# Performance work log

Measured on AMD Instinct MI355X. Metric: run time of the kernel, lower is better.

## Reference

```python
import jax, jax.numpy as jnp
import numpy as np
from jax import lax

KS = 3
PAD = 1


def setup_inputs() -> dict:
    key = jax.random.key(0)
    k1, k2, k3 = jax.random.split(key, 3)
    b, c, h, w = 8, 64, 128, 128
    out_c = 64
    x = jax.random.normal(k1, (b, c, h, w), dtype=jnp.float32)
    # small offset weights keep predicted offsets in a sane range
    w_off = jax.random.normal(k2, (2 * KS * KS, c, KS, KS), dtype=jnp.float32) * 0.05
    b_off = jnp.zeros((2 * KS * KS,), dtype=jnp.float32)
    w_reg = jax.random.normal(k3, (out_c, c * KS * KS), dtype=jnp.float32) * 0.02
    b_reg = jnp.zeros((out_c,), dtype=jnp.float32)
    return {"x": x, "w_off": w_off, "b_off": b_off, "w_reg": w_reg, "b_reg": b_reg}


def _deform_forward(x, w_off, b_off, w_reg, b_reg):
    ks, pad = KS, PAD
    b, c, h, w = x.shape
    # offset conv: 3x3, stride 1, pad 1 -> [b, 2*ks*ks, h, w]
    offset = lax.conv_general_dilated(
        x, w_off, window_strides=(1, 1), padding=[(pad, pad), (pad, pad)],
        dimension_numbers=("NCHW", "OIHW", "NCHW"))
    offset = offset + b_off[None, :, None, None]

    # pad input (zeros), as in the torch module
    xp = jnp.pad(x, ((0, 0), (0, 0), (pad, pad), (pad, pad)))
    Hp, Wp = h + 2 * pad, w + 2 * pad

    dt = x.dtype
    # base grid p0: [...,0] = column (x), [...,1] = row (y)
    yy, xx = jnp.meshgrid(jnp.arange(h, dtype=dt), jnp.arange(w, dtype=dt), indexing="ij")
    # kernel offsets p_n: flattened k = i*ks + j -> (lin[j], lin[i])
    lin = jnp.linspace(-(ks - 1) // 2, (ks - 1) // 2, ks).astype(dt)
    pn_i, pn_j = jnp.meshgrid(lin, lin, indexing="ij")
    pn = jnp.stack([pn_j, pn_i], axis=-1).reshape(ks * ks, 2)  # [ks2, 2]

    # offsets: [b, ks2, 2, h, w] -> [b, ks2, h, w, 2]; [...,0]=x off, [...,1]=y off
    off = offset.reshape(b, ks * ks, 2, h, w).transpose(0, 1, 3, 4, 2)

    px = xx[None, None] + pn[None, :, 0, None, None] + off[..., 0]  # [b, ks2, h, w]
    py = yy[None, None] + pn[None, :, 1, None, None] + off[..., 1]

    # torch normalizes by UNPADDED (w-1, h-1) but samples the PADDED tensor with
    # align_corners=True; reproduce exactly: q = p/(dim-1) * (dim_pad-1)
    qx = px / (w - 1) * (Wp - 1)
    qy = py / (h - 1) * (Hp - 1)

    x0 = jnp.floor(qx)
    y0 = jnp.floor(qy)
    wx1 = qx - x0  # frac weights
    wy1 = qy - y0
    wx0 = 1.0 - wx1
    wy0 = 1.0 - wy1
    ix0 = x0.astype(jnp.int32)
    iy0 = y0.astype(jnp.int32)
    ix1 = ix0 + 1
    iy1 = iy0 + 1

    def corner(iy, ix):
        valid = ((iy >= 0) & (iy < Hp) & (ix >= 0) & (ix < Wp)).astype(dt)
        iyc = jnp.clip(iy, 0, Hp - 1)
        ixc = jnp.clip(ix, 0, Wp - 1)
        # gather per batch: img [c,Hp,Wp], idx [ks2,h,w] -> [c,ks2,h,w]
        vals = jax.vmap(lambda img, a, bb: img[:, a, bb])(xp, iyc, ixc)
        return vals * valid[:, None]  # broadcast over channel dim

    v00 = corner(iy0, ix0)
    v01 = corner(iy0, ix1)
    v10 = corner(iy1, ix0)
    v11 = corner(iy1, ix1)

    wy0e = wy0[:, None]; wy1e = wy1[:, None]
    wx0e = wx0[:, None]; wx1e = wx1[:, None]
    sampled = (v00 * wy0e * wx0e + v01 * wy0e * wx1e +
               v10 * wy1e * wx0e + v11 * wy1e * wx1e)  # [b, c, ks2, h, w]

    # layout matches torch: [b, c*ks2, h, w] with (c, kk) order
    xs = sampled.reshape(b, c * ks * ks, h, w)
    out = jnp.einsum("bkhw,ok->bohw", xs, w_reg) + b_reg[None, :, None, None]
    return out


def reference(x, w_off, b_off, w_reg, b_reg):
    return _deform_forward(x, w_off, b_off, w_reg, b_reg)
```

## Files before the change

### kernel.cpp

```cpp
#include <hip/hip_runtime.h>
#include <math.h>

#define HH 128
#define WW 128
#define CC 64
#define BB 8
#define OC 64
#define OFFC 18
#define HW (HH*WW)
#define HP 136
#define WP 136
#define PHW (HP*WP)

typedef __attribute__((ext_vector_type(8))) _Float16 f16x8;
typedef __attribute__((ext_vector_type(4))) float f32x4;

#define P_OFF      0
#define P_SIZE     (BB*32*PHW)
#define OFFS_OFF   (P_OFF + P_SIZE)
#define OFFS_SIZE  (BB*OFFC*HW)
#define WAREG_OFF  (OFFS_OFF + OFFS_SIZE)
#define WAREG_SIZE 18432
#define WAOFF_OFF  (WAREG_OFF + WAREG_SIZE)

__device__ __forceinline__ unsigned short f2h(float f) {
    _Float16 t = (_Float16)f;
    unsigned short s;
    __builtin_memcpy(&s, &t, 2);
    return s;
}
__device__ __forceinline__ f16x8 u4_to_h8(uint4 u) {
    union { uint4 u; f16x8 h; } c; c.u = u; return c.h;
}
__device__ __forceinline__ uint4 h8_to_u4(f16x8 h) {
    union { uint4 u; f16x8 h; } c; c.h = h; return c.u;
}
__device__ __forceinline__ f16x8 splat8(float f) {
    _Float16 t = (_Float16)f;
    return (f16x8){t, t, t, t, t, t, t, t};
}

__global__ __launch_bounds__(256) void prep_kernel(
    const float* __restrict__ w_reg, const float* __restrict__ w_off,
    unsigned short* __restrict__ wA_reg, unsigned short* __restrict__ wA_off)
{
    int i = blockIdx.x * 256 + threadIdx.x;
    if (i < 18 * 64 * 32) {
        int j = i & 7, quad = (i >> 3) & 3, o = (i >> 5) & 63, ks = i >> 11;
        int kt = ks >> 1, kk = ks & 1;
        int c = kk * 32 + quad * 8 + j;
        wA_reg[i] = f2h(w_reg[o * 576 + c * 9 + kt]);
    }
    if (i < 18 * 32 * 32) {
        int j = i & 7, quad = (i >> 3) & 3, o = (i >> 5) & 31, ks = i >> 10;
        int kt = ks >> 1, kk = ks & 1;
        int c = kk * 32 + quad * 8 + j;
        float v = (o < OFFC) ? w_off[(o * CC + c) * 9 + kt] : 0.0f;
        wA_off[i] = f2h(v);
    }
}

__global__ __launch_bounds__(256) void pad_kernel(
    const float* __restrict__ x, uint4* __restrict__ P)
{
    int idx = blockIdx.x * 256 + threadIdx.x;
    if (idx >= BB * 8 * PHW) return;
    int pos = idx % PHW;
    int ig  = idx / PHW;
    int r   = pos / WP;
    int col = pos % WP;
    union { uint4 u; f16x8 h; } cv;
    cv.u = make_uint4(0u, 0u, 0u, 0u);
    if (r >= 4 && r <= 131 && col >= 4 && col <= 131) {
        const float* src = x + (ig * 8) * HW + (r - 4) * WW + (col - 4);
        #pragma unroll
        for (int e = 0; e < 8; ++e)
            cv.h[e] = (_Float16)src[e * HW];
    }
    P[idx] = cv.u;
}

__global__ __launch_bounds__(256) void offset_conv_kernel(
    const uint4* __restrict__ P, const unsigned short* __restrict__ wA_off,
    const float* __restrict__ b_off, float* __restrict__ offs)
{
    __shared__ uint4 xs[3 * 8 * 132];
    int img  = blockIdx.x & 7;
    int pblk = blockIdx.x >> 3;
    int tid  = threadIdx.x;
    const f16x8* wAv = (const f16x8*)wA_off;
    int lane = tid & 63;
    int wvid = tid >> 6;
    int s  = wvid & 1;
    int ph = wvid >> 1;

    for (int i = tid; i < 3 * 8 * 130; i += 256) {
        int r   = i / 1040;
        int rem = i - r * 1040;
        int g   = rem / 130;
        int j   = rem - g * 130;
        xs[(r * 8 + g) * 132 + j] =
            P[(img * 8 + g) * PHW + (pblk + 3 + r) * WP + (j + 3)];
    }
    __syncthreads();

    f32x4 acc[4];
    #pragma unroll
    for (int pt = 0; pt < 4; ++pt) acc[pt] = (f32x4){0.f, 0.f, 0.f, 0.f};

    const f16x8* xsv = (const f16x8*)xs;
    for (int tap = 0; tap < 9; ++tap) {
        int dy = tap / 3, dx = tap % 3;
        f16x8 a0 = wAv[((tap * 2 + 0) * 32 + s * 16 + (lane & 15)) * 4 + (lane >> 4)];
        f16x8 a1 = wAv[((tap * 2 + 1) * 32 + s * 16 + (lane & 15)) * 4 + (lane >> 4)];
        #pragma unroll
        for (int pt = 0; pt < 4; ++pt) {
            int j = ph * 64 + pt * 16 + (lane & 15) + dx;
            f16x8 b0 = xsv[(dy * 8 + (lane >> 4)) * 132 + j];
            acc[pt] = __builtin_amdgcn_mfma_f32_16x16x32_f16(a0, b0, acc[pt], 0, 0, 0);
            f16x8 b1 = xsv[(dy * 8 + 4 + (lane >> 4)) * 132 + j];
            acc[pt] = __builtin_amdgcn_mfma_f32_16x16x32_f16(a1, b1, acc[pt], 0, 0, 0);
        }
    }

    float* ob = offs + img * (OFFC * HW) + pblk * 128;
    #pragma unroll
    for (int r = 0; r < 4; ++r) {
        int o = s * 16 + (lane >> 4) * 4 + r;
        if (o < OFFC) {
            float bias = b_off[o];
            #pragma unroll
            for (int pt = 0; pt < 4; ++pt) {
                int pxl = ph * 64 + pt * 16 + (lane & 15);
                ob[o * HW + pxl] = acc[pt][r] + bias;
            }
        }
    }
}


struct Gather8 {
    uint4 a00, a01, a10, a11;
    uint4 b00, b01, b10, b11;
    float wx1, wy1;
};

__device__ __forceinline__ Gather8 issue_tap(
    const uint4* __restrict__ xq0, const uint4* __restrict__ xq1,
    int wv, int hv, int dx, int dy, float offx, float offy)
{
    const float scale = 129.0f / 127.0f;
    float pxf = ((float)wv + (float)dx) + offx;
    float pyf = ((float)hv + (float)dy) + offy;
    float qx = fminf(fmaxf(pxf * scale, -100.0f), 300.0f);
    float qy = fminf(fmaxf(pyf * scale, -100.0f), 300.0f);
    float x0f = floorf(qx), y0f = floorf(qy);
    Gather8 g;
    g.wx1 = qx - x0f;
    g.wy1 = qy - y0f;
    int ix0 = (int)x0f, iy0 = (int)y0f;
    int c0 = min(max(ix0 + 3, 0), WP - 2);
    int r0 = min(max(iy0 + 3, 0), HP - 1);
    int r1 = min(max(iy0 + 4, 0), HP - 1);
    int pr0 = r0 * WP + c0, pr1 = r1 * WP + c0;
    g.a00 = xq0[pr0]; g.a01 = xq0[pr0 + 1];
    g.a10 = xq0[pr1]; g.a11 = xq0[pr1 + 1];
    g.b00 = xq1[pr0]; g.b01 = xq1[pr0 + 1];
    g.b10 = xq1[pr1]; g.b11 = xq1[pr1 + 1];
    return g;
}

__device__ __forceinline__ void blend_write(
    uint4* __restrict__ dst, int qp, int pxl, const Gather8& g)
{
    f16x8 wx1v = splat8(g.wx1), wx0v = splat8(1.0f - g.wx1);
    f16x8 wy1v = splat8(g.wy1), wy0v = splat8(1.0f - g.wy1);
    f16x8 r0a = u4_to_h8(g.a00) * wx0v + u4_to_h8(g.a01) * wx1v;
    f16x8 r1a = u4_to_h8(g.a10) * wx0v + u4_to_h8(g.a11) * wx1v;
    dst[(qp * 2 + 0) * 64 + pxl] = h8_to_u4(r0a * wy0v + r1a * wy1v);
    f16x8 r0b = u4_to_h8(g.b00) * wx0v + u4_to_h8(g.b01) * wx1v;
    f16x8 r1b = u4_to_h8(g.b10) * wx0v + u4_to_h8(g.b11) * wx1v;
    dst[(qp * 2 + 1) * 64 + pxl] = h8_to_u4(r0b * wy0v + r1b * wy1v);
}

__global__ __launch_bounds__(256, 4) void deform_main_kernel(
    const uint4* __restrict__ P, const float* __restrict__ offs,
    const unsigned short* __restrict__ wA_reg, const float* __restrict__ b_reg,
    float* __restrict__ out)
{
    __shared__ uint4 xs2[2 * 512];
    int img  = blockIdx.x & 7;
    int rest = blockIdx.x >> 3;
    int half = rest & 1;
    int pblk = rest >> 1;
    int tid  = threadIdx.x;
    int pxl  = tid & 63;
    int qp   = tid >> 6;
    int wv = half * 64 + pxl;
    int hv = pblk;
    const float*  obf = offs + img * (OFFC * HW) + hv * WW + wv;
    const f16x8*  wAv = (const f16x8*)wA_reg;
    int lane = tid & 63;
    int wvid = tid >> 6;
    const uint4* xq0 = P + (img * 8 + qp * 2 + 0) * PHW;
    const uint4* xq1 = P + (img * 8 + qp * 2 + 1) * PHW;
    int aidx = (wvid * 16 + (lane & 15)) * 4 + (lane >> 4);

    f32x4 acc[4];
    #pragma unroll
    for (int pt = 0; pt < 4; ++pt) acc[pt] = (f32x4){0.f, 0.f, 0.f, 0.f};

    float ox0 = obf[0],      oy0 = obf[HW];
    float ox1 = obf[2 * HW], oy1 = obf[3 * HW];
    Gather8 cur = issue_tap(xq0, xq1, wv, hv, -1, -1, ox0, oy0);
    f16x8 a0c = wAv[0 * 64 * 4 + aidx];
    f16x8 a1c = wAv[1 * 64 * 4 + aidx];

    #pragma unroll
    for (int tap = 0; tap < 9; ++tap) {
        uint4* dst = xs2 + (tap & 1) * 512;
        blend_write(dst, qp, pxl, cur);

        float ox2 = 0.f, oy2 = 0.f;
        if (tap < 7) {
            ox2 = obf[(2 * tap + 4) * HW];
            oy2 = obf[(2 * tap + 5) * HW];
        }

        Gather8 nxt;
        f16x8 a0n, a1n;
        if (tap < 8) {
            int dx1 = (tap + 1) % 3 - 1, dy1 = (tap + 1) / 3 - 1;
            nxt = issue_tap(xq0, xq1, wv, hv, dx1, dy1, ox1, oy1);
            a0n = wAv[((tap + 1) * 2 + 0) * 64 * 4 + aidx];
            a1n = wAv[((tap + 1) * 2 + 1) * 64 * 4 + aidx];
        }

        asm volatile("s_waitcnt lgkmcnt(0)" ::: "memory");
        __builtin_amdgcn_s_barrier();
        asm volatile("" ::: "memory");

        const f16x8* xsv = (const f16x8*)(xs2 + (tap & 1) * 512);
        #pragma unroll
        for (int pt = 0; pt < 4; ++pt) {
            int pxi = pt * 16 + (lane & 15);
            f16x8 b0 = xsv[(lane >> 4) * 64 + pxi];
            acc[pt] = __builtin_amdgcn_mfma_f32_16x16x32_f16(a0c, b0, acc[pt], 0, 0, 0);
            f16x8 b1 = xsv[(4 + (lane >> 4)) * 64 + pxi];
            acc[pt] = __builtin_amdgcn_mfma_f32_16x16x32_f16(a1c, b1, acc[pt], 0, 0, 0);
        }

        if (tap < 8) {
            cur = nxt; a0c = a0n; a1c = a1n;
            ox1 = ox2; oy1 = oy2;
        }
    }

    float* op = out + img * (OC * HW) + hv * WW + half * 64;
    #pragma unroll
    for (int r = 0; r < 4; ++r) {
        int o = wvid * 16 + (lane >> 4) * 4 + r;
        float bias = b_reg[o];
        #pragma unroll
        for (int pt = 0; pt < 4; ++pt)
            op[o * HW + pt * 16 + (lane & 15)] = acc[pt][r] + bias;
    }
}

extern "C" void kernel_launch(void* const* d_in, const int* in_sizes, int n_in,
                              void* d_out, int out_size, void* d_ws, size_t ws_size,
                              hipStream_t stream) {
    const float* x     = (const float*)d_in[0];
    const float* w_off = (const float*)d_in[1];
    const float* b_off = (const float*)d_in[2];
    const float* w_reg = (const float*)d_in[3];
    const float* b_reg = (const float*)d_in[4];
    float* out = (float*)d_out;
    float* ws  = (float*)d_ws;

    uint4* P      = (uint4*)(ws + P_OFF);
    float* offs   = ws + OFFS_OFF;
    unsigned short* wA_reg = (unsigned short*)(ws + WAREG_OFF);
    unsigned short* wA_off = (unsigned short*)(ws + WAOFF_OFF);

    prep_kernel<<<144, 256, 0, stream>>>(w_reg, w_off, wA_reg, wA_off);
    pad_kernel<<<(BB * 8 * PHW + 255) / 256, 256, 0, stream>>>(x, P);
    offset_conv_kernel<<<1024, 256, 0, stream>>>(P, wA_off, b_off, offs);
    deform_main_kernel<<<2048, 256, 0, stream>>>(P, offs, wA_reg, b_reg, out);
}
```

Before: 155.1 us.

## Fuse offset conv into deform kernel and merge prep with pad kernel

Computes the offset convolution inside the deform kernel for each 64-pixel half-row, keeps the offsets in LDS and drops the global offs buffer. Also merges the weight-prep and pad kernels into a single launch. This removes two kernel launches and the global write and read of the offset tensor. In exchange each block stages its own input halo and does extra MFMA work with an added barrier, and LDS use per block goes up, which could limit occupancy.

```diff
diff --git a/kernel.cpp b/kernel.cpp
--- a/kernel.cpp
+++ b/kernel.cpp
@@ -23,6 +23,9 @@
 #define WAREG_SIZE 18432
 #define WAOFF_OFF  (WAREG_OFF + WAREG_SIZE)
 
+#define PAD_BLOCKS 4624
+#define PREP_BLOCKS 144
+
 __device__ __forceinline__ unsigned short f2h(float f) {
     _Float16 t = (_Float16)f;
     unsigned short s;
@@ -40,104 +43,45 @@
     return (f16x8){t, t, t, t, t, t, t, t};
 }
 
-__global__ __launch_bounds__(256) void prep_kernel(
+__global__ __launch_bounds__(256) void prep_pad_kernel(
+    const float* __restrict__ x, uint4* __restrict__ P,
     const float* __restrict__ w_reg, const float* __restrict__ w_off,
     unsigned short* __restrict__ wA_reg, unsigned short* __restrict__ wA_off)
 {
-    int i = blockIdx.x * 256 + threadIdx.x;
-    if (i < 18 * 64 * 32) {
-        int j = i & 7, quad = (i >> 3) & 3, o = (i >> 5) & 63, ks = i >> 11;
-        int kt = ks >> 1, kk = ks & 1;
-        int c = kk * 32 + quad * 8 + j;
-        wA_reg[i] = f2h(w_reg[o * 576 + c * 9 + kt]);
-    }
-    if (i < 18 * 32 * 32) {
-        int j = i & 7, quad = (i >> 3) & 3, o = (i >> 5) & 31, ks = i >> 10;
-        int kt = ks >> 1, kk = ks & 1;
-        int c = kk * 32 + quad * 8 + j;
-        float v = (o < OFFC) ? w_off[(o * CC + c) * 9 + kt] : 0.0f;
-        wA_off[i] = f2h(v);
-    }
-}
-
-__global__ __launch_bounds__(256) void pad_kernel(
-    const float* __restrict__ x, uint4* __restrict__ P)
-{
-    int idx = blockIdx.x * 256 + threadIdx.x;
-    if (idx >= BB * 8 * PHW) return;
-    int pos = idx % PHW;
-    int ig  = idx / PHW;
-    int r   = pos / WP;
-    int col = pos % WP;
-    union { uint4 u; f16x8 h; } cv;
-    cv.u = make_uint4(0u, 0u, 0u, 0u);
-    if (r >= 4 && r <= 131 && col >= 4 && col <= 131) {
-        const float* src = x + (ig * 8) * HW + (r - 4) * WW + (col - 4);
-        #pragma unroll
-        for (int e = 0; e < 8; ++e)
-            cv.h[e] = (_Float16)src[e * HW];
-    }
-    P[idx] = cv.u;
-}
-
-__global__ __launch_bounds__(256) void offset_conv_kernel(
-    const uint4* __restrict__ P, const unsigned short* __restrict__ wA_off,
-    const float* __restrict__ b_off, float* __restrict__ offs)
-{
-    __shared__ uint4 xs[3 * 8 * 132];
-    int img  = blockIdx.x & 7;
-    int pblk = blockIdx.x >> 3;
-    int tid  = threadIdx.x;
-    const f16x8* wAv = (const f16x8*)wA_off;
-    int lane = tid & 63;
-    int wvid = tid >> 6;
-    int s  = wvid & 1;
-    int ph = wvid >> 1;
-
-    for (int i = tid; i < 3 * 8 * 130; i += 256) {
-        int r   = i / 1040;
-        int rem = i - r * 1040;
-        int g   = rem / 130;
-        int j   = rem - g * 130;
-        xs[(r * 8 + g) * 132 + j] =
-            P[(img * 8 + g) * PHW + (pblk + 3 + r) * WP + (j + 3)];
-    }
-    __syncthreads();
-
-    f32x4 acc[4];
-    #pragma unroll
-    for (int pt = 0; pt < 4; ++pt) acc[pt] = (f32x4){0.f, 0.f, 0.f, 0.f};
-
-    const f16x8* xsv = (const f16x8*)xs;
-    for (int tap = 0; tap < 9; ++tap) {
-        int dy = tap / 3, dx = tap % 3;
-        f16x8 a0 = wAv[((tap * 2 + 0) * 32 + s * 16 + (lane & 15)) * 4 + (lane >> 4)];
-        f16x8 a1 = wAv[((tap * 2 + 1) * 32 + s * 16 + (lane & 15)) * 4 + (lane >> 4)];
-        #pragma unroll
-        for (int pt = 0; pt < 4; ++pt) {
-            int j = ph * 64 + pt * 16 + (lane & 15) + dx;
-            f16x8 b0 = xsv[(dy * 8 + (lane >> 4)) * 132 + j];
-            acc[pt] = __builtin_amdgcn_mfma_f32_16x16x32_f16(a0, b0, acc[pt], 0, 0, 0);
-            f16x8 b1 = xsv[(dy * 8 + 4 + (lane >> 4)) * 132 + j];
-            acc[pt] = __builtin_amdgcn_mfma_f32_16x16x32_f16(a1, b1, acc[pt], 0, 0, 0);
-        }
-    }
-
-    float* ob = offs + img * (OFFC * HW) + pblk * 128;
-    #pragma unroll
-    for (int r = 0; r < 4; ++r) {
-        int o = s * 16 + (lane >> 4) * 4 + r;
-        if (o < OFFC) {
-            float bias = b_off[o];
+    int bid = blockIdx.x;
+    int tid = threadIdx.x;
+    if (bid < PAD_BLOCKS) {
+        int idx = bid * 256 + tid;
+        int pos = idx % PHW;
+        int ig  = idx / PHW;
+        int r   = pos / WP;
+        int col = pos % WP;
+        union { uint4 u; f16x8 h; } cv;
+        cv.u = make_uint4(0u, 0u, 0u, 0u);
+        if (r >= 4 && r <= 131 && col >= 4 && col <= 131) {
+            const float* src = x + (ig * 8) * HW + (r - 4) * WW + (col - 4);
             #pragma unroll
-            for (int pt = 0; pt < 4; ++pt) {
-                int pxl = ph * 64 + pt * 16 + (lane & 15);
-                ob[o * HW + pxl] = acc[pt][r] + bias;
-            }
-        }
-    }
-}
-
+            for (int e = 0; e < 8; ++e)
+                cv.h[e] = (_Float16)src[e * HW];
+        }
+        P[idx] = cv.u;
+    } else {
+        int i = (bid - PAD_BLOCKS) * 256 + tid;
+        if (i < 18 * 64 * 32) {
+            int j = i & 7, quad = (i >> 3) & 3, o = (i >> 5) & 63, ks = i >> 11;
+            int kt = ks >> 1, kk = ks & 1;
+            int c = kk * 32 + quad * 8 + j;
+            wA_reg[i] = f2h(w_reg[o * 576 + c * 9 + kt]);
+        }
+        if (i < 18 * 32 * 32) {
+            int j = i & 7, quad = (i >> 3) & 3, o = (i >> 5) & 31, ks = i >> 10;
+            int kt = ks >> 1, kk = ks & 1;
+            int c = kk * 32 + quad * 8 + j;
+            float v = (o < OFFC) ? w_off[(o * CC + c) * 9 + kt] : 0.0f;
+            wA_off[i] = f2h(v);
+        }
+    }
+}
 
 struct Gather8 {
     uint4 a00, a01, a10, a11;
@@ -183,12 +127,13 @@
     dst[(qp * 2 + 1) * 64 + pxl] = h8_to_u4(r0b * wy0v + r1b * wy1v);
 }
 
-__global__ __launch_bounds__(256, 4) void deform_main_kernel(
-    const uint4* __restrict__ P, const float* __restrict__ offs,
-    const unsigned short* __restrict__ wA_reg, const float* __restrict__ b_reg,
-    float* __restrict__ out)
-{
-    __shared__ uint4 xs2[2 * 512];
+__global__ __launch_bounds__(256, 4) void fused_deform_kernel(
+    const uint4* __restrict__ P, const unsigned short* __restrict__ wA_off,
+    const float* __restrict__ b_off, const unsigned short* __restrict__ wA_reg,
+    const float* __restrict__ b_reg, float* __restrict__ out)
+{
+    __shared__ uint4 shbuf[3 * 8 * 66];
+    __shared__ float offs_lds[OFFC * 64];
     int img  = blockIdx.x & 7;
     int rest = blockIdx.x >> 3;
     int half = rest & 1;
@@ -196,12 +141,58 @@
     int tid  = threadIdx.x;
     int pxl  = tid & 63;
     int qp   = tid >> 6;
+    int lane = tid & 63;
+    int wvid = tid >> 6;
     int wv = half * 64 + pxl;
     int hv = pblk;
-    const float*  obf = offs + img * (OFFC * HW) + hv * WW + wv;
-    const f16x8*  wAv = (const f16x8*)wA_reg;
-    int lane = tid & 63;
-    int wvid = tid >> 6;
+
+    for (int i = tid; i < 3 * 8 * 66; i += 256) {
+        int r   = i / 528;
+        int rem = i - r * 528;
+        int g   = rem / 66;
+        int j   = rem - g * 66;
+        shbuf[(r * 8 + g) * 66 + j] =
+            P[(img * 8 + g) * PHW + (pblk + 3 + r) * WP + (half * 64 + 3 + j)];
+    }
+    __syncthreads();
+
+    {
+        int s2  = wvid & 1;
+        int ph2 = wvid >> 1;
+        const f16x8* wOv = (const f16x8*)wA_off;
+        const f16x8* xsc = (const f16x8*)shbuf;
+        f32x4 oacc[2];
+        oacc[0] = (f32x4){0.f, 0.f, 0.f, 0.f};
+        oacc[1] = (f32x4){0.f, 0.f, 0.f, 0.f};
+        for (int tap = 0; tap < 9; ++tap) {
+            int dy = tap / 3, dx = tap % 3;
+            f16x8 a0 = wOv[((tap * 2 + 0) * 32 + s2 * 16 + (lane & 15)) * 4 + (lane >> 4)];
+            f16x8 a1 = wOv[((tap * 2 + 1) * 32 + s2 * 16 + (lane & 15)) * 4 + (lane >> 4)];
+            #pragma unroll
+            for (int pt = 0; pt < 2; ++pt) {
+                int sj = ph2 * 32 + pt * 16 + (lane & 15) + dx;
+                f16x8 b0 = xsc[(dy * 8 + (lane >> 4)) * 66 + sj];
+                oacc[pt] = __builtin_amdgcn_mfma_f32_16x16x32_f16(a0, b0, oacc[pt], 0, 0, 0);
+                f16x8 b1 = xsc[(dy * 8 + 4 + (lane >> 4)) * 66 + sj];
+                oacc[pt] = __builtin_amdgcn_mfma_f32_16x16x32_f16(a1, b1, oacc[pt], 0, 0, 0);
+            }
+        }
+        #pragma unroll
+        for (int r = 0; r < 4; ++r) {
+            int o = s2 * 16 + (lane >> 4) * 4 + r;
+            if (o < OFFC) {
+                float bias = b_off[o];
+                #pragma unroll
+                for (int pt = 0; pt < 2; ++pt) {
+                    int p = ph2 * 32 + pt * 16 + (lane & 15);
+                    offs_lds[o * 64 + p] = oacc[pt][r] + bias;
+                }
+            }
+        }
+    }
+    __syncthreads();
+
+    const f16x8* wAv = (const f16x8*)wA_reg;
     const uint4* xq0 = P + (img * 8 + qp * 2 + 0) * PHW;
     const uint4* xq1 = P + (img * 8 + qp * 2 + 1) * PHW;
     int aidx = (wvid * 16 + (lane & 15)) * 4 + (lane >> 4);
@@ -210,37 +201,32 @@
     #pragma unroll
     for (int pt = 0; pt < 4; ++pt) acc[pt] = (f32x4){0.f, 0.f, 0.f, 0.f};
 
-    float ox0 = obf[0],      oy0 = obf[HW];
-    float ox1 = obf[2 * HW], oy1 = obf[3 * HW];
-    Gather8 cur = issue_tap(xq0, xq1, wv, hv, -1, -1, ox0, oy0);
-    f16x8 a0c = wAv[0 * 64 * 4 + aidx];
-    f16x8 a1c = wAv[1 * 64 * 4 + aidx];
+    float ox = offs_lds[0 * 64 + pxl], oy = offs_lds[1 * 64 + pxl];
+    Gather8 cur = issue_tap(xq0, xq1, wv, hv, -1, -1, ox, oy);
+    f16x8 a0c = wAv[0 * 256 + aidx];
+    f16x8 a1c = wAv[1 * 256 + aidx];
 
     #pragma unroll
     for (int tap = 0; tap < 9; ++tap) {
-        uint4* dst = xs2 + (tap & 1) * 512;
+        uint4* dst = shbuf + (tap & 1) * 512;
         blend_write(dst, qp, pxl, cur);
-
-        float ox2 = 0.f, oy2 = 0.f;
-        if (tap < 7) {
-            ox2 = obf[(2 * tap + 4) * HW];
-            oy2 = obf[(2 * tap + 5) * HW];
-        }
 
         Gather8 nxt;
         f16x8 a0n, a1n;
         if (tap < 8) {
             int dx1 = (tap + 1) % 3 - 1, dy1 = (tap + 1) / 3 - 1;
-            nxt = issue_tap(xq0, xq1, wv, hv, dx1, dy1, ox1, oy1);
-            a0n = wAv[((tap + 1) * 2 + 0) * 64 * 4 + aidx];
-            a1n = wAv[((tap + 1) * 2 + 1) * 64 * 4 + aidx];
+            float oxn = offs_lds[(2 * tap + 2) * 64 + pxl];
+            float oyn = offs_lds[(2 * tap + 3) * 64 + pxl];
+            nxt = issue_tap(xq0, xq1, wv, hv, dx1, dy1, oxn, oyn);
+            a0n = wAv[((tap + 1) * 2 + 0) * 256 + aidx];
+            a1n = wAv[((tap + 1) * 2 + 1) * 256 + aidx];
         }
 
         asm volatile("s_waitcnt lgkmcnt(0)" ::: "memory");
         __builtin_amdgcn_s_barrier();
         asm volatile("" ::: "memory");
 
-        const f16x8* xsv = (const f16x8*)(xs2 + (tap & 1) * 512);
+        const f16x8* xsv = (const f16x8*)(shbuf + (tap & 1) * 512);
         #pragma unroll
         for (int pt = 0; pt < 4; ++pt) {
             int pxi = pt * 16 + (lane & 15);
@@ -252,7 +238,6 @@
 
         if (tap < 8) {
             cur = nxt; a0c = a0n; a1c = a1n;
-            ox1 = ox2; oy1 = oy2;
         }
     }
 
@@ -279,12 +264,11 @@
     float* ws  = (float*)d_ws;
 
     uint4* P      = (uint4*)(ws + P_OFF);
-    float* offs   = ws + OFFS_OFF;
     unsigned short* wA_reg = (unsigned short*)(ws + WAREG_OFF);
     unsigned short* wA_off = (unsigned short*)(ws + WAOFF_OFF);
 
-    prep_kernel<<<144, 256, 0, stream>>>(w_reg, w_off, wA_reg, wA_off);
-    pad_kernel<<<(BB * 8 * PHW + 255) / 256, 256, 0, stream>>>(x, P);
-    offset_conv_kernel<<<1024, 256, 0, stream>>>(P, wA_off, b_off, offs);
-    deform_main_kernel<<<2048, 256, 0, stream>>>(P, offs, wA_reg, b_reg, out);
-}
+    prep_pad_kernel<<<PAD_BLOCKS + PREP_BLOCKS, 256, 0, stream>>>(
+        x, P, w_reg, w_off, wA_reg, wA_off);
+    fused_deform_kernel<<<2048, 256, 0, stream>>>(
+        P, wA_off, b_off, wA_reg, b_reg, out);
+}
```

After: 145.2 us. -6.4%, faster.
